# Optimization experiments

Hardware: AMD Instinct MI355X
Metric: run time of the kernel (lower is better)

The kernel has to match this reference:

```python
import jax, jax.numpy as jnp
import numpy as np

N = 50000      # nodes
E = 800000     # edges
D_IN = 256     # state_dim
H = 128        # HIDDEN_LAYER
A = 32         # action_dim
EPS = 1e-5
NEG_SLOPE = 0.2


def setup_inputs() -> dict:
    key = jax.random.key(0)
    ks = jax.random.split(key, 16)
    s = lambda k, shape, std=0.1: jax.random.normal(k, shape, jnp.float32) * std
    return {
        "x": jax.random.normal(ks[0], (N, D_IN), jnp.float32),
        "edge_index": jax.random.randint(ks[1], (2, E), 0, N, jnp.int64),
        # GAT params
        "W": s(ks[2], (D_IN, H)),
        "a_src": s(ks[3], (H,)),
        "a_dst": s(ks[4], (H,)),
        "b_gat": jnp.zeros((H,), jnp.float32),
        # bn0
        "g0": jnp.ones((H,), jnp.float32),
        "beta0": jnp.zeros((H,), jnp.float32),
        # fc1, fc2
        "W1": s(ks[5], (H, H)),
        "b1": jnp.zeros((H,), jnp.float32),
        "W2": s(ks[6], (H, H)),
        "b2": jnp.zeros((H,), jnp.float32),
        # bn2
        "g2": jnp.ones((H,), jnp.float32),
        "beta2": jnp.zeros((H,), jnp.float32),
        # fc3
        "W3": s(ks[7], (H, A)),
        "b3": jnp.zeros((A,), jnp.float32),
    }


def _batchnorm(h, gamma, beta):
    # training-mode BN: biased batch stats over node dim
    mu = jnp.mean(h, axis=0)
    var = jnp.var(h, axis=0)
    return (h - mu) * jax.lax.rsqrt(var + EPS) * gamma + beta


def _gat(x, edge_index, W, a_src, a_dst, b_gat):
    src, dst = edge_index[0], edge_index[1]
    h = x @ W                                  # [N, H]
    e_src = h @ a_src                          # [N]
    e_dst = h @ a_dst                          # [N]
    e = jax.nn.leaky_relu(e_src[src] + e_dst[dst], NEG_SLOPE)  # [E]
    # neighbor softmax over edges grouped by destination node
    m = jax.ops.segment_max(e, dst, num_segments=N)            # [N]
    w = jnp.exp(e - m[dst])                                    # [E]
    denom = jax.ops.segment_sum(w, dst, num_segments=N)        # [N]
    alpha = w / jnp.maximum(denom, 1e-16)[dst]                 # [E]
    out = jax.ops.segment_sum(alpha[:, None] * h[src], dst, num_segments=N)
    return out + b_gat


def reference(x, edge_index, W, a_src, a_dst, b_gat, g0, beta0,
              W1, b1, W2, b2, g2, beta2, W3, b3):
    h0 = jax.nn.relu(_gat(x, edge_index, W, a_src, a_dst, b_gat))
    h0n = _batchnorm(h0, g0, beta0)
    h1 = jax.nn.relu(h0n @ W1 + b1)
    h2 = jax.nn.relu(h1 @ W2 + b2)
    h2n = _batchnorm(h2, g2, beta2)
    action = h2n @ W3 + b3
    return jax.nn.softmax(action, axis=1)
```

## Files before the change

### kernel.cpp

```cpp
#include <hip/hip_runtime.h>
#include <math.h>

#define N_NODES 50000
#define N_EDGES 800000
#define D_INPUT 256
#define HDIM 128
#define A_DIM 32
#define NEG_SLOPE 0.2f
#define BN_EPS 1e-5f
#define CAP 64
#define NB 391
#define BIN_SHIFT 7
#define BCAP 2432
#define GC_STRIDE 16
#define EPB 4096
#define FC3_TR 64
#define SROW 132

typedef short short8 __attribute__((ext_vector_type(8)));
typedef unsigned short ushort8v __attribute__((ext_vector_type(8)));
typedef unsigned short ushort4v __attribute__((ext_vector_type(4)));
typedef float float4v __attribute__((ext_vector_type(4)));

__device__ __forceinline__ unsigned short f2bf(float f) {
  unsigned u = __float_as_uint(f);
  u += 0x7FFFu + ((u >> 16) & 1u);
  return (unsigned short)(u >> 16);
}
__device__ __forceinline__ float bf2f(unsigned short b) {
  return __uint_as_float(((unsigned)b) << 16);
}

__device__ __forceinline__ float waveReduceMax(float v) {
#pragma unroll
  for (int o = 32; o >= 1; o >>= 1) v = fmaxf(v, __shfl_xor(v, o, 64));
  return v;
}
__device__ __forceinline__ float waveReduceSum(float v) {
#pragma unroll
  for (int o = 32; o >= 1; o >>= 1) v += __shfl_xor(v, o, 64);
  return v;
}

__global__ __launch_bounds__(256) void k_prep(
    const float* __restrict__ W, const float* __restrict__ W1,
    const float* __restrict__ W2, unsigned short* __restrict__ Wt0,
    unsigned short* __restrict__ Wt1, unsigned short* __restrict__ Wt2,
    int* __restrict__ gcur, float* __restrict__ stats)
{
  int i = blockIdx.x * 256 + threadIdx.x;
  if (i < HDIM * D_INPUT) {
    int n = i >> 8, k = i & 255;
    Wt0[i] = f2bf(W[(size_t)k * HDIM + n]);
  }
  if (i < HDIM * HDIM) {
    int n = i >> 7, k = i & 127;
    Wt1[i] = f2bf(W1[(size_t)k * HDIM + n]);
    Wt2[i] = f2bf(W2[(size_t)k * HDIM + n]);
  }
  if (i < NB * GC_STRIDE) gcur[i] = 0;
  if (i < 512) stats[i] = 0.f;
}

__global__ __launch_bounds__(256) void k_gemmbin(
    const float* __restrict__ x, const unsigned short* __restrict__ Wt0,
    const float* __restrict__ a_src, const float* __restrict__ a_dst,
    unsigned short* __restrict__ hbf, float* __restrict__ esrc, float* __restrict__ edst,
    const int* __restrict__ srcI, const int* __restrict__ dstI,
    int* __restrict__ gcur, int* __restrict__ bbuf)
{
  const int gT = (N_NODES + 63) / 64;
  __shared__ short As[64][72];
  __shared__ short Bs[128][72];
  __shared__ float esred[64][2], edred[64][2];
  __shared__ int hist[NB];
  __shared__ int base[NB];

  const int t = threadIdx.x;

  if (blockIdx.x >= gT) {
    const int e0 = (blockIdx.x - gT) * EPB;
    const int e1 = min(e0 + EPB, N_EDGES);
    for (int i = t; i < NB; i += 256) hist[i] = 0;
    __syncthreads();
    for (int e = e0 + t; e < e1; e += 256)
      atomicAdd(&hist[dstI[e] >> BIN_SHIFT], 1);
    __syncthreads();
    for (int i = t; i < NB; i += 256) {
      base[i] = atomicAdd(&gcur[i * GC_STRIDE], hist[i]);
      hist[i] = 0;
    }
    __syncthreads();
    for (int e = e0 + t; e < e1; e += 256) {
      int d = dstI[e];
      int bin = d >> BIN_SHIFT;
      int r = atomicAdd(&hist[bin], 1) + base[bin];
      if (r < BCAP) bbuf[(size_t)bin * BCAP + r] = srcI[e] | ((d & 127) << 16);
    }
    return;
  }

  const int lane = t & 63;
  const int wv = t >> 6;
  const int rh = wv >> 1;
  const int ch = wv & 1;
  const int quad = (lane >> 4) & 3;
  const int l15 = lane & 15;
  const int row0 = blockIdx.x * 64;

  float4v acc[2][4];
#pragma unroll
  for (int i = 0; i < 2; ++i)
#pragma unroll
    for (int j = 0; j < 4; ++j) acc[i][j] = (float4v){0.f, 0.f, 0.f, 0.f};

  for (int ks = 0; ks < D_INPUT / 64; ++ks) {
    const int kk0 = ks * 64;
#pragma unroll
    for (int it = 0; it < 4; ++it) {
      int idx = it * 256 + t;
      int r = idx >> 4, c4 = idx & 15;
      int rr = row0 + r; if (rr >= N_NODES) rr = N_NODES - 1;
      float4 v = *(const float4*)(x + (size_t)rr * D_INPUT + kk0 + c4 * 4);
      ushort4v b; b.x = f2bf(v.x); b.y = f2bf(v.y); b.z = f2bf(v.z); b.w = f2bf(v.w);
      *(ushort4v*)(&As[r][c4 * 4]) = b;
    }
#pragma unroll
    for (int it = 0; it < 4; ++it) {
      int idx = it * 256 + t;
      int n = idx >> 3, c8 = idx & 7;
      *(ushort8v*)(&Bs[n][c8 * 8]) = *(const ushort8v*)(Wt0 + (size_t)n * D_INPUT + kk0 + c8 * 8);
    }
    __syncthreads();
#pragma unroll
    for (int kc = 0; kc < 2; ++kc) {
      short8 af[2], bfr[4];
#pragma unroll
      for (int rt = 0; rt < 2; ++rt)
        af[rt] = *(const short8*)(&As[rh * 32 + rt * 16 + l15][kc * 32 + quad * 8]);
#pragma unroll
      for (int nt = 0; nt < 4; ++nt)
        bfr[nt] = *(const short8*)(&Bs[ch * 64 + nt * 16 + l15][kc * 32 + quad * 8]);
#pragma unroll
      for (int rt = 0; rt < 2; ++rt)
#pragma unroll
        for (int nt = 0; nt < 4; ++nt)
          acc[rt][nt] = __builtin_amdgcn_mfma_f32_16x16x32_bf16(af[rt], bfr[nt], acc[rt][nt], 0, 0, 0);
    }
    __syncthreads();
  }

  float asv[4], adv[4];
#pragma unroll
  for (int nt = 0; nt < 4; ++nt) {
    int col = ch * 64 + nt * 16 + l15;
    asv[nt] = a_src[col]; adv[nt] = a_dst[col];
  }
#pragma unroll
  for (int rt = 0; rt < 2; ++rt) {
#pragma unroll
    for (int reg = 0; reg < 4; ++reg) {
      int rloc = rh * 32 + rt * 16 + quad * 4 + reg;
      int row = row0 + rloc;
      bool valid = (row < N_NODES);
      float ps = 0.f, pd = 0.f;
#pragma unroll
      for (int nt = 0; nt < 4; ++nt) {
        float v = acc[rt][nt][reg];
        ps += v * asv[nt]; pd += v * adv[nt];
        if (valid) hbf[(size_t)row * HDIM + ch * 64 + nt * 16 + l15] = f2bf(v);
      }
#pragma unroll
      for (int o = 8; o >= 1; o >>= 1) {
        ps += __shfl_xor(ps, o, 64);
        pd += __shfl_xor(pd, o, 64);
      }
      if (l15 == 0) { esred[rloc][ch] = ps; edred[rloc][ch] = pd; }
    }
  }
  __syncthreads();
  if (t < 64) {
    int row = row0 + t;
    if (row < N_NODES) {
      esrc[row] = esred[t][0] + esred[t][1];
      edst[row] = edred[t][0] + edred[t][1];
    }
  }
}

__global__ __launch_bounds__(256) void k_sc2(
    const int* __restrict__ gcur, const int* __restrict__ bbuf,
    const float* __restrict__ esrc, const float* __restrict__ edst,
    int* __restrict__ deg, int2* __restrict__ sedge)
{
  __shared__ int2 bk[128][CAP];
  __shared__ int lcur[128];
  __shared__ float ledst[128];
  const int t = threadIdx.x;
  const int bin = blockIdx.x;
  const int d0 = bin << BIN_SHIFT;
  if (t < 128) {
    lcur[t] = 0;
    int d = d0 + t;
    ledst[t] = (d < N_NODES) ? edst[d] : 0.f;
  }
  __syncthreads();
  const int cnt = min(gcur[bin * GC_STRIDE], BCAP);
  const int* seg = bbuf + (size_t)bin * BCAP;
  for (int i = t; i < cnt; i += 256) {
    int v = seg[i];
    int s = v & 0xFFFF;
    int dl = (v >> 16) & 127;
    float ev = esrc[s] + ledst[dl];
    ev = (ev > 0.f) ? ev : NEG_SLOPE * ev;
    int r = atomicAdd(&lcur[dl], 1);
    if (r < CAP) {
      int2 e2; e2.x = s; e2.y = __float_as_int(ev);
      bk[dl][r] = e2;
    }
  }
  __syncthreads();
  for (int idx = t; idx < 128 * CAP; idx += 256) {
    int dl = idx >> 6, sl = idx & 63;
    if (sl < lcur[dl])
      sedge[(size_t)(d0 + dl) * CAP + sl] = bk[dl][sl];
  }
  if (t < 128) {
    int d = d0 + t;
    if (d < N_NODES) deg[d] = min(lcur[t], CAP);
  }
}

__global__ __launch_bounds__(256) void k_agg(
    const int* __restrict__ degA, const int2* __restrict__ sedge,
    const unsigned short* __restrict__ hbf,
    const float* __restrict__ b_gat, unsigned short* __restrict__ h0)
{
  const int t = threadIdx.x;
  const int lane = t & 63;
  const int node = blockIdx.x * 4 + (t >> 6);
  const int deg = min(degA[node], CAP);

  int2 ev; ev.x = 0; ev.y = 0;
  float val = -INFINITY;
  if (lane < deg) {
    ev = sedge[(size_t)node * CAP + lane];
    val = __int_as_float(ev.y);
  }
  const float m = waveReduceMax(val);
  const float ex = (lane < deg) ? __expf(val - m) : 0.f;
  const float s = waveReduceSum(ex);
  const float al = ex * (1.0f / fmaxf(s, 1e-16f));
  const int sr = ev.x;

  float ax = 0.f, ay = 0.f;
  int j = 0;
  for (; j + 4 <= deg; j += 4) {
    float a0 = __shfl(al, j, 64),   a1 = __shfl(al, j+1, 64);
    float a2 = __shfl(al, j+2, 64), a3 = __shfl(al, j+3, 64);
    int s0 = __shfl(sr, j, 64),   s1 = __shfl(sr, j+1, 64);
    int s2 = __shfl(sr, j+2, 64), s3 = __shfl(sr, j+3, 64);
    unsigned v0 = *(const unsigned*)(hbf + (size_t)s0 * HDIM + lane * 2);
    unsigned v1 = *(const unsigned*)(hbf + (size_t)s1 * HDIM + lane * 2);
    unsigned v2 = *(const unsigned*)(hbf + (size_t)s2 * HDIM + lane * 2);
    unsigned v3 = *(const unsigned*)(hbf + (size_t)s3 * HDIM + lane * 2);
    ax += a0 * bf2f((unsigned short)(v0 & 0xFFFFu))
        + a1 * bf2f((unsigned short)(v1 & 0xFFFFu))
        + a2 * bf2f((unsigned short)(v2 & 0xFFFFu))
        + a3 * bf2f((unsigned short)(v3 & 0xFFFFu));
    ay += a0 * bf2f((unsigned short)(v0 >> 16))
        + a1 * bf2f((unsigned short)(v1 >> 16))
        + a2 * bf2f((unsigned short)(v2 >> 16))
        + a3 * bf2f((unsigned short)(v3 >> 16));
  }
  for (; j < deg; ++j) {
    float a = __shfl(al, j, 64);
    int sj = __shfl(sr, j, 64);
    unsigned v = *(const unsigned*)(hbf + (size_t)sj * HDIM + lane * 2);
    ax += a * bf2f((unsigned short)(v & 0xFFFFu));
    ay += a * bf2f((unsigned short)(v >> 16));
  }
  float vx = fmaxf(ax + b_gat[lane * 2], 0.f);
  float vy = fmaxf(ay + b_gat[lane * 2 + 1], 0.f);
  *(unsigned*)(h0 + (size_t)node * HDIM + lane * 2) =
      (unsigned)f2bf(vx) | ((unsigned)f2bf(vy) << 16);
}

#define BN_ROWS 256
__global__ __launch_bounds__(256) void k_bnstats(
    const unsigned short* __restrict__ src, float* __restrict__ gsum, float* __restrict__ gsq)
{
  __shared__ float red[16][128];
  const int t = threadIdx.x;
  const int cg = t & 15;
  const int rl = t >> 4;
  const int row0 = blockIdx.x * BN_ROWS;
  float s[8], q[8];
#pragma unroll
  for (int j = 0; j < 8; ++j) { s[j] = 0.f; q[j] = 0.f; }
  for (int i = 0; i < BN_ROWS / 16; ++i) {
    int row = row0 + rl + i * 16;
    if (row < N_NODES) {
      ushort8v v = *(const ushort8v*)(src + (size_t)row * HDIM + cg * 8);
#pragma unroll
      for (int j = 0; j < 8; ++j) {
        float f = bf2f(v[j]);
        s[j] += f; q[j] += f * f;
      }
    }
  }
#pragma unroll
  for (int j = 0; j < 8; ++j) red[rl][cg * 8 + j] = s[j];
  __syncthreads();
  if (t < 128) {
    float S = 0.f;
#pragma unroll
    for (int r = 0; r < 16; ++r) S += red[r][t];
    atomicAdd(&gsum[t], S);
  }
  __syncthreads();
#pragma unroll
  for (int j = 0; j < 8; ++j) red[rl][cg * 8 + j] = q[j];
  __syncthreads();
  if (t < 128) {
    float Q = 0.f;
#pragma unroll
    for (int r = 0; r < 16; ++r) Q += red[r][t];
    atomicAdd(&gsq[t], Q);
  }
}

__global__ __launch_bounds__(256) void k_fc12(
    const unsigned short* __restrict__ in,
    const float* __restrict__ gsumIn, const float* __restrict__ gsqIn,
    const float* __restrict__ gamma, const float* __restrict__ beta,
    const unsigned short* __restrict__ Wt1, const float* __restrict__ b1,
    const unsigned short* __restrict__ Wt2, const float* __restrict__ b2,
    unsigned short* __restrict__ outp,
    float* __restrict__ gsum, float* __restrict__ gsq)
{
  __shared__ short As[64 * SROW];
  __shared__ short Bsh[128 * SROW];
  __shared__ float statS[128][2], statQ[128][2];
  __shared__ float sc[HDIM], shf[HDIM];

  const int t = threadIdx.x;
  const int lane = t & 63;
  const int wv = t >> 6;
  const int rh = wv >> 1;
  const int ch = wv & 1;
  const int quad = (lane >> 4) & 3;
  const int l15 = lane & 15;
  const int row0 = blockIdx.x * 64;

  if (t < HDIM) {
    float mean = gsumIn[t] / (float)N_NODES;
    float var = gsqIn[t] / (float)N_NODES - mean * mean;
    float s = gamma[t] * rsqrtf(var + BN_EPS);
    sc[t] = s; shf[t] = beta[t] - mean * s;
  }
  __syncthreads();

#pragma unroll
  for (int it = 0; it < 4; ++it) {
    int idx = it * 256 + t;
    int r = idx >> 4, c8 = idx & 15;
    int rr = row0 + r; if (rr >= N_NODES) rr = N_NODES - 1;
    ushort8v v = *(const ushort8v*)(in + (size_t)rr * HDIM + c8 * 8);
#pragma unroll
    for (int j = 0; j < 8; ++j) {
      int k = c8 * 8 + j;
      v[j] = f2bf(bf2f(v[j]) * sc[k] + shf[k]);
    }
    *(ushort8v*)(&As[r * SROW + c8 * 8]) = v;
  }
#pragma unroll
  for (int it = 0; it < 8; ++it) {
    int idx = it * 256 + t;
    int n = idx >> 4, c8 = idx & 15;
    *(ushort8v*)(&Bsh[n * SROW + c8 * 8]) = *(const ushort8v*)(Wt1 + (size_t)n * HDIM + c8 * 8);
  }
  __syncthreads();

  float4v acc[2][4];
#pragma unroll
  for (int i = 0; i < 2; ++i)
#pragma unroll
    for (int j = 0; j < 4; ++j) acc[i][j] = (float4v){0.f, 0.f, 0.f, 0.f};

#pragma unroll
  for (int kc = 0; kc < 4; ++kc) {
    short8 af[2], bfr[4];
#pragma unroll
    for (int rt = 0; rt < 2; ++rt)
      af[rt] = *(const short8*)(&As[(rh * 32 + rt * 16 + l15) * SROW + kc * 32 + quad * 8]);
#pragma unroll
    for (int nt = 0; nt < 4; ++nt)
      bfr[nt] = *(const short8*)(&Bsh[(ch * 64 + nt * 16 + l15) * SROW + kc * 32 + quad * 8]);
#pragma unroll
    for (int rt = 0; rt < 2; ++rt)
#pragma unroll
      for (int nt = 0; nt < 4; ++nt)
        acc[rt][nt] = __builtin_amdgcn_mfma_f32_16x16x32_bf16(af[rt], bfr[nt], acc[rt][nt], 0, 0, 0);
  }
  __syncthreads();

  {
    float bv[4];
#pragma unroll
    for (int nt = 0; nt < 4; ++nt) bv[nt] = b1[ch * 64 + nt * 16 + l15];
#pragma unroll
    for (int rt = 0; rt < 2; ++rt) {
#pragma unroll
      for (int reg = 0; reg < 4; ++reg) {
        int rloc = rh * 32 + rt * 16 + quad * 4 + reg;
#pragma unroll
        for (int nt = 0; nt < 4; ++nt) {
          float o = fmaxf(acc[rt][nt][reg] + bv[nt], 0.f);
          As[rloc * SROW + ch * 64 + nt * 16 + l15] = f2bf(o);
        }
      }
    }
  }
#pragma unroll
  for (int it = 0; it < 8; ++it) {
    int idx = it * 256 + t;
    int n = idx >> 4, c8 = idx & 15;
    *(ushort8v*)(&Bsh[n * SROW + c8 * 8]) = *(const ushort8v*)(Wt2 + (size_t)n * HDIM + c8 * 8);
  }
  __syncthreads();

#pragma unroll
  for (int i = 0; i < 2; ++i)
#pragma unroll
    for (int j = 0; j < 4; ++j) acc[i][j] = (float4v){0.f, 0.f, 0.f, 0.f};

#pragma unroll
  for (int kc = 0; kc < 4; ++kc) {
    short8 af[2], bfr[4];
#pragma unroll
    for (int rt = 0; rt < 2; ++rt)
      af[rt] = *(const short8*)(&As[(rh * 32 + rt * 16 + l15) * SROW + kc * 32 + quad * 8]);
#pragma unroll
    for (int nt = 0; nt < 4; ++nt)
      bfr[nt] = *(const short8*)(&Bsh[(ch * 64 + nt * 16 + l15) * SROW + kc * 32 + quad * 8]);
#pragma unroll
    for (int rt = 0; rt < 2; ++rt)
#pragma unroll
      for (int nt = 0; nt < 4; ++nt)
        acc[rt][nt] = __builtin_amdgcn_mfma_f32_16x16x32_bf16(af[rt], bfr[nt], acc[rt][nt], 0, 0, 0);
  }

  float bv[4];
#pragma unroll
  for (int nt = 0; nt < 4; ++nt) bv[nt] = b2[ch * 64 + nt * 16 + l15];

  float pS[4] = {0.f, 0.f, 0.f, 0.f}, pQ[4] = {0.f, 0.f, 0.f, 0.f};
#pragma unroll
  for (int rt = 0; rt < 2; ++rt) {
#pragma unroll
    for (int reg = 0; reg < 4; ++reg) {
      int row = row0 + rh * 32 + rt * 16 + quad * 4 + reg;
      bool valid = (row < N_NODES);
#pragma unroll
      for (int nt = 0; nt < 4; ++nt) {
        float o = fmaxf(acc[rt][nt][reg] + bv[nt], 0.f);
        if (valid) {
          outp[(size_t)row * HDIM + ch * 64 + nt * 16 + l15] = f2bf(o);
          pS[nt] += o; pQ[nt] += o * o;
        }
      }
    }
  }
#pragma unroll
  for (int nt = 0; nt < 4; ++nt) {
    float s = pS[nt], q = pQ[nt];
    s += __shfl_xor(s, 16, 64); s += __shfl_xor(s, 32, 64);
    q += __shfl_xor(q, 16, 64); q += __shfl_xor(q, 32, 64);
    if (lane < 16) {
      statS[ch * 64 + nt * 16 + lane][rh] = s;
      statQ[ch * 64 + nt * 16 + lane][rh] = q;
    }
  }
  __syncthreads();
  if (t < 128) {
    atomicAdd(&gsum[t], statS[t][0] + statS[t][1]);
    atomicAdd(&gsq[t],  statQ[t][0] + statQ[t][1]);
  }
}

__global__ __launch_bounds__(128) void k_fc3(
    const unsigned short* __restrict__ h2,
    const float* __restrict__ gsumIn, const float* __restrict__ gsqIn,
    const float* __restrict__ gamma, const float* __restrict__ beta,
    const float* __restrict__ W3, const float* __restrict__ b3,
    float* __restrict__ out)
{
  __shared__ float w3p[HDIM][A_DIM];
  __shared__ float hs[HDIM][FC3_TR + 2];
  __shared__ float s2s[HDIM], sh2s[HDIM];
  __shared__ float bred[4][A_DIM];
  __shared__ float b3p[A_DIM];
  const int t = threadIdx.x;

  {
    float mean = gsumIn[t] / (float)N_NODES;
    float var = gsqIn[t] / (float)N_NODES - mean * mean;
    float s = gamma[t] * rsqrtf(var + BN_EPS);
    s2s[t] = s; sh2s[t] = beta[t] - mean * s;
  }
  __syncthreads();

  for (int i = t; i < HDIM * A_DIM; i += 128) {
    int k = i >> 5;
    w3p[k][i & 31] = s2s[k] * W3[i];
  }
  {
    int j = t & 31, seg = t >> 5;
    float p = 0.f;
    for (int kk = 0; kk < 32; ++kk) {
      int k = seg * 32 + kk;
      p += sh2s[k] * W3[k * A_DIM + j];
    }
    bred[seg][j] = p;
  }
  const int row0 = blockIdx.x * FC3_TR;
  for (int i = t; i < FC3_TR * (HDIM / 8); i += 128) {
    int r = i & 63, cg = i >> 6;
    int row = row0 + r;
    ushort8v v;
    if (row < N_NODES) v = *(const ushort8v*)(h2 + (size_t)row * HDIM + cg * 8);
    else { for (int jj = 0; jj < 8; ++jj) v[jj] = 0; }
#pragma unroll
    for (int jj = 0; jj < 8; ++jj) hs[cg * 8 + jj][r] = bf2f(v[jj]);
  }
  __syncthreads();
  if (t < 32) b3p[t] = b3[t] + bred[0][t] + bred[1][t] + bred[2][t] + bred[3][t];
  __syncthreads();

  const int r0 = (t >> 3) * 4;
  const int j0 = (t & 7) * 4;
  float4 acc[4];
#pragma unroll
  for (int r = 0; r < 4; ++r) acc[r] = (float4){0.f, 0.f, 0.f, 0.f};

  for (int k = 0; k < HDIM; k += 4) {
    float4 w0 = *(const float4*)&w3p[k + 0][j0];
    float4 w1 = *(const float4*)&w3p[k + 1][j0];
    float4 w2 = *(const float4*)&w3p[k + 2][j0];
    float4 w3v = *(const float4*)&w3p[k + 3][j0];
#pragma unroll
    for (int r = 0; r < 4; ++r) {
      int rr = r0 + r;
      float h0 = hs[k + 0][rr], h1 = hs[k + 1][rr];
      float h2v = hs[k + 2][rr], h3 = hs[k + 3][rr];
      acc[r].x += h0 * w0.x + h1 * w1.x + h2v * w2.x + h3 * w3v.x;
      acc[r].y += h0 * w0.y + h1 * w1.y + h2v * w2.y + h3 * w3v.y;
      acc[r].z += h0 * w0.z + h1 * w1.z + h2v * w2.z + h3 * w3v.z;
      acc[r].w += h0 * w0.w + h1 * w1.w + h2v * w2.w + h3 * w3v.w;
    }
  }

  float4 b4 = *(const float4*)&b3p[j0];
#pragma unroll
  for (int r = 0; r < 4; ++r) {
    float l0 = acc[r].x + b4.x, l1 = acc[r].y + b4.y;
    float l2 = acc[r].z + b4.z, l3 = acc[r].w + b4.w;
    float mx = fmaxf(fmaxf(l0, l1), fmaxf(l2, l3));
#pragma unroll
    for (int o = 1; o <= 4; o <<= 1) mx = fmaxf(mx, __shfl_xor(mx, o, 64));
    float e0 = __expf(l0 - mx), e1 = __expf(l1 - mx);
    float e2 = __expf(l2 - mx), e3 = __expf(l3 - mx);
    float sm = e0 + e1 + e2 + e3;
#pragma unroll
    for (int o = 1; o <= 4; o <<= 1) sm += __shfl_xor(sm, o, 64);
    float inv = 1.0f / sm;
    int row = row0 + r0 + r;
    if (row < N_NODES) {
      float4 o4; o4.x = e0 * inv; o4.y = e1 * inv; o4.z = e2 * inv; o4.w = e3 * inv;
      *(float4*)(out + (size_t)row * A_DIM + j0) = o4;
    }
  }
}

extern "C" void kernel_launch(void* const* d_in, const int* in_sizes, int n_in,
                              void* d_out, int out_size, void* d_ws, size_t ws_size,
                              hipStream_t stream) {
  const float* x     = (const float*)d_in[0];
  const int*   ei    = (const int*)d_in[1];
  const float* W     = (const float*)d_in[2];
  const float* a_src = (const float*)d_in[3];
  const float* a_dst = (const float*)d_in[4];
  const float* b_gat = (const float*)d_in[5];
  const float* g0    = (const float*)d_in[6];
  const float* beta0 = (const float*)d_in[7];
  const float* W1    = (const float*)d_in[8];
  const float* b1    = (const float*)d_in[9];
  const float* W2    = (const float*)d_in[10];
  const float* b2    = (const float*)d_in[11];
  const float* g2    = (const float*)d_in[12];
  const float* beta2 = (const float*)d_in[13];
  const float* W3    = (const float*)d_in[14];
  const float* b3    = (const float*)d_in[15];
  float* out = (float*)d_out;
  const int* srcI = ei;
  const int* dstI = ei + N_EDGES;

  char* p = (char*)d_ws;
  auto alloc = [&](size_t bytes) -> char* {
    char* q = p; p += (bytes + 255) & ~(size_t)255; return q;
  };
  unsigned short* h   = (unsigned short*)alloc(sizeof(short) * (size_t)N_NODES * HDIM);
  unsigned short* h0  = (unsigned short*)alloc(sizeof(short) * (size_t)N_NODES * HDIM);
  unsigned short* h2  = h;
  unsigned short* Wt0 = (unsigned short*)alloc(sizeof(short) * HDIM * D_INPUT);
  unsigned short* Wt1 = (unsigned short*)alloc(sizeof(short) * HDIM * HDIM);
  unsigned short* Wt2 = (unsigned short*)alloc(sizeof(short) * HDIM * HDIM);
  int2*  sedge  = (int2*)alloc(sizeof(int2) * (size_t)N_NODES * CAP);
  int*   bbuf   = (int*)alloc(sizeof(int) * (size_t)NB * BCAP);
  float* esrc   = (float*)alloc(sizeof(float) * N_NODES);
  float* edst   = (float*)alloc(sizeof(float) * N_NODES);
  int*   deg    = (int*)alloc(sizeof(int) * N_NODES);
  int*   gcur   = (int*)alloc(sizeof(int) * NB * GC_STRIDE);
  float* stats  = (float*)alloc(sizeof(float) * 4 * 128);
  float* gsum0 = stats;        float* gsq0  = stats + 128;
  float* gsum2 = stats + 256;  float* gsq2  = stats + 384;

  const int gT = (N_NODES + 63) / 64;
  const int gB = (N_EDGES + EPB - 1) / EPB;
  const int gP = (HDIM * D_INPUT + 255) / 256;

  k_prep<<<gP, 256, 0, stream>>>(W, W1, W2, Wt0, Wt1, Wt2, gcur, stats);
  k_gemmbin<<<gT + gB, 256, 0, stream>>>(x, Wt0, a_src, a_dst, h, esrc, edst,
                                         srcI, dstI, gcur, bbuf);
  k_sc2<<<NB, 256, 0, stream>>>(gcur, bbuf, esrc, edst, deg, sedge);
  k_agg<<<N_NODES / 4, 256, 0, stream>>>(deg, sedge, h, b_gat, h0);
  k_bnstats<<<(N_NODES + BN_ROWS - 1) / BN_ROWS, 256, 0, stream>>>(h0, gsum0, gsq0);
  k_fc12<<<gT, 256, 0, stream>>>(h0, gsum0, gsq0, g0, beta0, Wt1, b1, Wt2, b2, h2,
                                 gsum2, gsq2);
  k_fc3<<<(N_NODES + FC3_TR - 1) / FC3_TR, 128, 0, stream>>>(
      h2, gsum2, gsq2, g2, beta2, W3, b3, out);
}
```

Measured before the change: 248.4 us.

## Fuse edge scatter, GAT aggregation and BN0 statistics into one kernel

Merges the per-bin edge bucketing, the softmax-weighted neighbor aggregation and the first batchnorm statistics pass into a single 512-thread kernel per destination bin. Edge buckets stay in shared memory instead of being written to a global sedge/deg array and read back, and BN sums are accumulated from registers rather than re-reading h0. The cost is far less parallelism: only 391 blocks, each with 8 waves that process 16 nodes serially, so the latency of the gather loads may be poorly hidden on a GPU with many CUs.

```diff
diff --git a/kernel.cpp b/kernel.cpp
--- a/kernel.cpp
+++ b/kernel.cpp
@@ -188,17 +188,22 @@
   }
 }
 
-__global__ __launch_bounds__(256) void k_sc2(
+__global__ __launch_bounds__(512) void k_scagg(
     const int* __restrict__ gcur, const int* __restrict__ bbuf,
     const float* __restrict__ esrc, const float* __restrict__ edst,
-    int* __restrict__ deg, int2* __restrict__ sedge)
+    const unsigned short* __restrict__ hbf, const float* __restrict__ b_gat,
+    unsigned short* __restrict__ h0,
+    float* __restrict__ gsum, float* __restrict__ gsq)
 {
   __shared__ int2 bk[128][CAP];
   __shared__ int lcur[128];
   __shared__ float ledst[128];
+  __shared__ float redS[8][128];
+  __shared__ float redQ[8][128];
   const int t = threadIdx.x;
   const int bin = blockIdx.x;
   const int d0 = bin << BIN_SHIFT;
+
   if (t < 128) {
     lcur[t] = 0;
     int d = d0 + t;
@@ -207,125 +212,87 @@
   __syncthreads();
   const int cnt = min(gcur[bin * GC_STRIDE], BCAP);
   const int* seg = bbuf + (size_t)bin * BCAP;
-  for (int i = t; i < cnt; i += 256) {
+  for (int i = t; i < cnt; i += 512) {
     int v = seg[i];
     int s = v & 0xFFFF;
     int dl = (v >> 16) & 127;
-    float ev = esrc[s] + ledst[dl];
-    ev = (ev > 0.f) ? ev : NEG_SLOPE * ev;
+    float evv = esrc[s] + ledst[dl];
+    evv = (evv > 0.f) ? evv : NEG_SLOPE * evv;
     int r = atomicAdd(&lcur[dl], 1);
     if (r < CAP) {
-      int2 e2; e2.x = s; e2.y = __float_as_int(ev);
+      int2 e2; e2.x = s; e2.y = __float_as_int(evv);
       bk[dl][r] = e2;
     }
   }
   __syncthreads();
-  for (int idx = t; idx < 128 * CAP; idx += 256) {
-    int dl = idx >> 6, sl = idx & 63;
-    if (sl < lcur[dl])
-      sedge[(size_t)(d0 + dl) * CAP + sl] = bk[dl][sl];
-  }
+
+  const int lane = t & 63;
+  const int wv = t >> 6;
+  const float bgx = b_gat[lane * 2], bgy = b_gat[lane * 2 + 1];
+  float sx = 0.f, sy = 0.f, qx = 0.f, qy = 0.f;
+
+  for (int i = 0; i < 16; ++i) {
+    const int dl = wv * 16 + i;
+    const int node = d0 + dl;
+    const int deg = min(lcur[dl], CAP);
+
+    int2 ev; ev.x = 0; ev.y = 0;
+    float val = -INFINITY;
+    if (lane < deg) {
+      ev = bk[dl][lane];
+      val = __int_as_float(ev.y);
+    }
+    const float m = waveReduceMax(val);
+    const float ex = (lane < deg) ? __expf(val - m) : 0.f;
+    const float s = waveReduceSum(ex);
+    const float al = ex * (1.0f / fmaxf(s, 1e-16f));
+    const int sr = ev.x;
+
+    float ax = 0.f, ay = 0.f;
+    int j = 0;
+    for (; j + 4 <= deg; j += 4) {
+      float a0 = __shfl(al, j, 64),   a1 = __shfl(al, j+1, 64);
+      float a2 = __shfl(al, j+2, 64), a3 = __shfl(al, j+3, 64);
+      int s0 = __shfl(sr, j, 64),   s1 = __shfl(sr, j+1, 64);
+      int s2 = __shfl(sr, j+2, 64), s3 = __shfl(sr, j+3, 64);
+      unsigned v0 = *(const unsigned*)(hbf + (size_t)s0 * HDIM + lane * 2);
+      unsigned v1 = *(const unsigned*)(hbf + (size_t)s1 * HDIM + lane * 2);
+      unsigned v2 = *(const unsigned*)(hbf + (size_t)s2 * HDIM + lane * 2);
+      unsigned v3 = *(const unsigned*)(hbf + (size_t)s3 * HDIM + lane * 2);
+      ax += a0 * bf2f((unsigned short)(v0 & 0xFFFFu))
+          + a1 * bf2f((unsigned short)(v1 & 0xFFFFu))
+          + a2 * bf2f((unsigned short)(v2 & 0xFFFFu))
+          + a3 * bf2f((unsigned short)(v3 & 0xFFFFu));
+      ay += a0 * bf2f((unsigned short)(v0 >> 16))
+          + a1 * bf2f((unsigned short)(v1 >> 16))
+          + a2 * bf2f((unsigned short)(v2 >> 16))
+          + a3 * bf2f((unsigned short)(v3 >> 16));
+    }
+    for (; j < deg; ++j) {
+      float a = __shfl(al, j, 64);
+      int sj = __shfl(sr, j, 64);
+      unsigned v = *(const unsigned*)(hbf + (size_t)sj * HDIM + lane * 2);
+      ax += a * bf2f((unsigned short)(v & 0xFFFFu));
+      ay += a * bf2f((unsigned short)(v >> 16));
+    }
+    float vx = fmaxf(ax + bgx, 0.f);
+    float vy = fmaxf(ay + bgy, 0.f);
+    if (node < N_NODES) {
+      *(unsigned*)(h0 + (size_t)node * HDIM + lane * 2) =
+          (unsigned)f2bf(vx) | ((unsigned)f2bf(vy) << 16);
+      sx += vx; qx += vx * vx;
+      sy += vy; qy += vy * vy;
+    }
+  }
+
+  redS[wv][lane * 2] = sx; redS[wv][lane * 2 + 1] = sy;
+  redQ[wv][lane * 2] = qx; redQ[wv][lane * 2 + 1] = qy;
+  __syncthreads();
   if (t < 128) {
-    int d = d0 + t;
-    if (d < N_NODES) deg[d] = min(lcur[t], CAP);
-  }
-}
-
-__global__ __launch_bounds__(256) void k_agg(
-    const int* __restrict__ degA, const int2* __restrict__ sedge,
-    const unsigned short* __restrict__ hbf,
-    const float* __restrict__ b_gat, unsigned short* __restrict__ h0)
-{
-  const int t = threadIdx.x;
-  const int lane = t & 63;
-  const int node = blockIdx.x * 4 + (t >> 6);
-  const int deg = min(degA[node], CAP);
-
-  int2 ev; ev.x = 0; ev.y = 0;
-  float val = -INFINITY;
-  if (lane < deg) {
-    ev = sedge[(size_t)node * CAP + lane];
-    val = __int_as_float(ev.y);
-  }
-  const float m = waveReduceMax(val);
-  const float ex = (lane < deg) ? __expf(val - m) : 0.f;
-  const float s = waveReduceSum(ex);
-  const float al = ex * (1.0f / fmaxf(s, 1e-16f));
-  const int sr = ev.x;
-
-  float ax = 0.f, ay = 0.f;
-  int j = 0;
-  for (; j + 4 <= deg; j += 4) {
-    float a0 = __shfl(al, j, 64),   a1 = __shfl(al, j+1, 64);
-    float a2 = __shfl(al, j+2, 64), a3 = __shfl(al, j+3, 64);
-    int s0 = __shfl(sr, j, 64),   s1 = __shfl(sr, j+1, 64);
-    int s2 = __shfl(sr, j+2, 64), s3 = __shfl(sr, j+3, 64);
-    unsigned v0 = *(const unsigned*)(hbf + (size_t)s0 * HDIM + lane * 2);
-    unsigned v1 = *(const unsigned*)(hbf + (size_t)s1 * HDIM + lane * 2);
-    unsigned v2 = *(const unsigned*)(hbf + (size_t)s2 * HDIM + lane * 2);
-    unsigned v3 = *(const unsigned*)(hbf + (size_t)s3 * HDIM + lane * 2);
-    ax += a0 * bf2f((unsigned short)(v0 & 0xFFFFu))
-        + a1 * bf2f((unsigned short)(v1 & 0xFFFFu))
-        + a2 * bf2f((unsigned short)(v2 & 0xFFFFu))
-        + a3 * bf2f((unsigned short)(v3 & 0xFFFFu));
-    ay += a0 * bf2f((unsigned short)(v0 >> 16))
-        + a1 * bf2f((unsigned short)(v1 >> 16))
-        + a2 * bf2f((unsigned short)(v2 >> 16))
-        + a3 * bf2f((unsigned short)(v3 >> 16));
-  }
-  for (; j < deg; ++j) {
-    float a = __shfl(al, j, 64);
-    int sj = __shfl(sr, j, 64);
-    unsigned v = *(const unsigned*)(hbf + (size_t)sj * HDIM + lane * 2);
-    ax += a * bf2f((unsigned short)(v & 0xFFFFu));
-    ay += a * bf2f((unsigned short)(v >> 16));
-  }
-  float vx = fmaxf(ax + b_gat[lane * 2], 0.f);
-  float vy = fmaxf(ay + b_gat[lane * 2 + 1], 0.f);
-  *(unsigned*)(h0 + (size_t)node * HDIM + lane * 2) =
-      (unsigned)f2bf(vx) | ((unsigned)f2bf(vy) << 16);
-}
-
-#define BN_ROWS 256
-__global__ __launch_bounds__(256) void k_bnstats(
-    const unsigned short* __restrict__ src, float* __restrict__ gsum, float* __restrict__ gsq)
-{
-  __shared__ float red[16][128];
-  const int t = threadIdx.x;
-  const int cg = t & 15;
-  const int rl = t >> 4;
-  const int row0 = blockIdx.x * BN_ROWS;
-  float s[8], q[8];
-#pragma unroll
-  for (int j = 0; j < 8; ++j) { s[j] = 0.f; q[j] = 0.f; }
-  for (int i = 0; i < BN_ROWS / 16; ++i) {
-    int row = row0 + rl + i * 16;
-    if (row < N_NODES) {
-      ushort8v v = *(const ushort8v*)(src + (size_t)row * HDIM + cg * 8);
-#pragma unroll
-      for (int j = 0; j < 8; ++j) {
-        float f = bf2f(v[j]);
-        s[j] += f; q[j] += f * f;
-      }
-    }
-  }
-#pragma unroll
-  for (int j = 0; j < 8; ++j) red[rl][cg * 8 + j] = s[j];
-  __syncthreads();
-  if (t < 128) {
-    float S = 0.f;
-#pragma unroll
-    for (int r = 0; r < 16; ++r) S += red[r][t];
+    float S = 0.f, Q = 0.f;
+#pragma unroll
+    for (int w = 0; w < 8; ++w) { S += redS[w][t]; Q += redQ[w][t]; }
     atomicAdd(&gsum[t], S);
-  }
-  __syncthreads();
-#pragma unroll
-  for (int j = 0; j < 8; ++j) red[rl][cg * 8 + j] = q[j];
-  __syncthreads();
-  if (t < 128) {
-    float Q = 0.f;
-#pragma unroll
-    for (int r = 0; r < 16; ++r) Q += red[r][t];
     atomicAdd(&gsq[t], Q);
   }
 }
@@ -616,11 +583,9 @@
   unsigned short* Wt0 = (unsigned short*)alloc(sizeof(short) * HDIM * D_INPUT);
   unsigned short* Wt1 = (unsigned short*)alloc(sizeof(short) * HDIM * HDIM);
   unsigned short* Wt2 = (unsigned short*)alloc(sizeof(short) * HDIM * HDIM);
-  int2*  sedge  = (int2*)alloc(sizeof(int2) * (size_t)N_NODES * CAP);
   int*   bbuf   = (int*)alloc(sizeof(int) * (size_t)NB * BCAP);
   float* esrc   = (float*)alloc(sizeof(float) * N_NODES);
   float* edst   = (float*)alloc(sizeof(float) * N_NODES);
-  int*   deg    = (int*)alloc(sizeof(int) * N_NODES);
   int*   gcur   = (int*)alloc(sizeof(int) * NB * GC_STRIDE);
   float* stats  = (float*)alloc(sizeof(float) * 4 * 128);
   float* gsum0 = stats;        float* gsq0  = stats + 128;
@@ -633,9 +598,8 @@
   k_prep<<<gP, 256, 0, stream>>>(W, W1, W2, Wt0, Wt1, Wt2, gcur, stats);
   k_gemmbin<<<gT + gB, 256, 0, stream>>>(x, Wt0, a_src, a_dst, h, esrc, edst,
                                          srcI, dstI, gcur, bbuf);
-  k_sc2<<<NB, 256, 0, stream>>>(gcur, bbuf, esrc, edst, deg, sedge);
-  k_agg<<<N_NODES / 4, 256, 0, stream>>>(deg, sedge, h, b_gat, h0);
-  k_bnstats<<<(N_NODES + BN_ROWS - 1) / BN_ROWS, 256, 0, stream>>>(h0, gsum0, gsq0);
+  k_scagg<<<NB, 512, 0, stream>>>(gcur, bbuf, esrc, edst, h, b_gat, h0,
+                                  gsum0, gsq0);
   k_fc12<<<gT, 256, 0, stream>>>(h0, gsum0, gsq0, g0, beta0, Wt1, b1, Wt2, b2, h2,
                                  gsum2, gsq2);
   k_fc3<<<(N_NODES + FC3_TR - 1) / FC3_TR, 128, 0, stream>>>(
```

New measurement: 247.9 us. About the same (-0.2%).
